# Kernel optimization log

Hardware: AMD Instinct MI355X
Metric: run time of the kernel (lower is better)

## Reference

```python
import math
import jax, jax.numpy as jnp
from jax import lax
import numpy as np

N_IMG = 2
C = 128
IMG_H, IMG_W = 512, 1024
STRIDES = (4, 8, 16, 32, 64)
SIZES = (32.0, 64.0, 128.0, 256.0, 512.0)
RATIOS = (0.5, 1.0, 2.0)
A = len(RATIOS)
PRE_NMS_TOPK = 2000    # pre_nms_topk[self.training] with training=True
POST_NMS_TOPK = 1000   # post_nms_topk[self.training]
NMS_THRESH = 0.7
BATCH_PER_IMG = 256
POS_FRAC = 0.5
MIN_BOX_SIZE = 0.0
SCALE_CLAMP = math.log(1000.0 / 16.0)
MATCH_LOW, MATCH_HIGH = 0.3, 0.7


def cell_anchors(size):
    rs = jnp.asarray(RATIOS, jnp.float32)
    area = size * size
    w = jnp.sqrt(area / rs)
    h = w * rs
    return jnp.stack([-w / 2, -h / 2, w / 2, h / 2], axis=1)  # [A,4]


def level_anchors(H, W, stride, size):
    ca = cell_anchors(size)
    sx = jnp.arange(W, dtype=jnp.float32) * stride
    sy = jnp.arange(H, dtype=jnp.float32) * stride
    yy, xx = jnp.meshgrid(sy, sx, indexing="ij")
    shifts = jnp.stack([xx, yy, xx, yy], axis=-1).reshape(-1, 4)  # [H*W,4]
    return (shifts[:, None, :] + ca[None, :, :]).reshape(-1, 4)  # [H*W*A,4]


def pairwise_iou(a, b):
    lt = jnp.maximum(a[:, None, :2], b[None, :, :2])
    rb = jnp.minimum(a[:, None, 2:], b[None, :, 2:])
    wh = jnp.clip(rb - lt, 0.0)
    inter = wh[..., 0] * wh[..., 1]
    area_a = (a[:, 2] - a[:, 0]) * (a[:, 3] - a[:, 1])
    area_b = (b[:, 2] - b[:, 0]) * (b[:, 3] - b[:, 1])
    union = area_a[:, None] + area_b[None, :] - inter
    return jnp.where(inter > 0, inter / union, 0.0)


def get_deltas(src, tgt):
    sw = src[..., 2] - src[..., 0]; sh = src[..., 3] - src[..., 1]
    scx = src[..., 0] + 0.5 * sw;   scy = src[..., 1] + 0.5 * sh
    tw = tgt[..., 2] - tgt[..., 0]; th = tgt[..., 3] - tgt[..., 1]
    tcx = tgt[..., 0] + 0.5 * tw;   tcy = tgt[..., 1] + 0.5 * th
    return jnp.stack([(tcx - scx) / sw, (tcy - scy) / sh,
                      jnp.log(tw / sw), jnp.log(th / sh)], axis=-1)


def apply_deltas(deltas, boxes):
    w = boxes[..., 2] - boxes[..., 0]; h = boxes[..., 3] - boxes[..., 1]
    cx = boxes[..., 0] + 0.5 * w;      cy = boxes[..., 1] + 0.5 * h
    dx, dy = deltas[..., 0], deltas[..., 1]
    dw = jnp.minimum(deltas[..., 2], SCALE_CLAMP)
    dh = jnp.minimum(deltas[..., 3], SCALE_CLAMP)
    pcx = dx * w + cx; pcy = dy * h + cy
    pw = jnp.exp(dw) * w; ph = jnp.exp(dh) * h
    return jnp.stack([pcx - 0.5 * pw, pcy - 0.5 * ph,
                      pcx + 0.5 * pw, pcy + 0.5 * ph], axis=-1)


def conv(x, w, b):
    y = lax.conv_general_dilated(x, w, (1, 1), "SAME",
                                 dimension_numbers=("NCHW", "OIHW", "NCHW"))
    return y + b[None, :, None, None]


def rpn_forward_flat(feats, conv_w, conv_b, obj_w, obj_b, delta_w, delta_b):
    anchors, logits, deltas = [], [], []
    for (stride, size), f in zip(zip(STRIDES, SIZES), feats):
        N, _, H, W = f.shape
        h = jax.nn.relu(conv(f, conv_w, conv_b))
        lg = conv(h, obj_w, obj_b)       # [N,A,H,W]
        dl = conv(h, delta_w, delta_b)   # [N,4A,H,W]
        logits.append(lg.transpose(0, 2, 3, 1).reshape(N, -1))                     # [N,HWA]
        deltas.append(dl.reshape(N, A, 4, H, W).transpose(0, 3, 4, 1, 2).reshape(N, -1, 4))
        anchors.append(level_anchors(H, W, stride, size))
    return anchors, logits, deltas


def label_and_sample(gt_b, key, anchors_all):
    iou = pairwise_iou(gt_b, anchors_all)                 # [G,R]
    matched_idxs = jnp.argmax(iou, axis=0)
    matched_vals = jnp.max(iou, axis=0)
    labels = jnp.where(matched_vals >= MATCH_HIGH, 1,
             jnp.where(matched_vals >= MATCH_LOW, -1, 0))
    highest = jnp.max(iou, axis=1)                        # per-gt best IoU
    lq = jnp.any((iou == highest[:, None]) & (highest[:, None] > 0), axis=0)
    labels = jnp.where(lq, 1, labels)                     # allow_low_quality_matches
    R = labels.shape[0]
    kf, kb = jax.random.split(key)
    fg = labels == 1; bg = labels == 0
    num_fg = jnp.minimum(fg.sum(), int(POS_FRAC * BATCH_PER_IMG))
    num_bg = jnp.minimum(bg.sum(), BATCH_PER_IMG - num_fg)
    def pick(mask, k, num):
        pri = jnp.where(mask, jax.random.uniform(k, (R,)), jnp.inf)
        rank = jnp.argsort(jnp.argsort(pri))
        return rank < num
    sel_fg = pick(fg, kf, num_fg)
    sel_bg = pick(bg, kb, num_bg)
    labels = jnp.where(sel_fg, 1, jnp.where(sel_bg, 0, -1))
    return labels, gt_b[matched_idxs]


def losses_fn(anchors_all, logits_cat, deltas_cat, gt_labels, matched_gt):
    fg = (gt_labels == 1).astype(logits_cat.dtype)          # [N,R]
    gt_deltas = get_deltas(anchors_all[None], matched_gt)   # [N,R,4]
    loc = jnp.sum(jnp.abs(deltas_cat - gt_deltas) * fg[..., None])  # smooth_l1, beta=0
    valid = (gt_labels >= 0).astype(logits_cat.dtype)
    x = logits_cat
    bce = jnp.maximum(x, 0.0) - x * fg + jnp.log1p(jnp.exp(-jnp.abs(x)))
    cls = jnp.sum(bce * valid)
    norm = float(BATCH_PER_IMG) * logits_cat.shape[0]
    return jnp.stack([cls / norm, loc / norm])


def nms_keep(boxes, valid):
    # boxes are sorted by descending score; greedy suppression.
    K = boxes.shape[0]
    iou = pairwise_iou(boxes, boxes)
    idx = jnp.arange(K)
    def body(i, keep):
        sup = (iou[i] > NMS_THRESH) & (idx > i) & keep[i]
        return keep & ~sup
    return lax.fori_loop(0, K, body, valid)


def predict_proposals(anchors, logits, deltas):
    lvl_boxes, lvl_scores = [], []
    for anc, lg, dl in zip(anchors, logits, deltas):
        boxes = apply_deltas(dl, anc[None])             # [N,R_l,4]
        k = min(PRE_NMS_TOPK, lg.shape[1])
        ts, ti = lax.top_k(lg, k)                       # [N,k]
        tb = jnp.take_along_axis(boxes, ti[..., None], axis=1)
        tb = jnp.stack([jnp.clip(tb[..., 0], 0.0, IMG_W), jnp.clip(tb[..., 1], 0.0, IMG_H),
                        jnp.clip(tb[..., 2], 0.0, IMG_W), jnp.clip(tb[..., 3], 0.0, IMG_H)], -1)
        valid = ((tb[..., 2] - tb[..., 0]) > MIN_BOX_SIZE) & ((tb[..., 3] - tb[..., 1]) > MIN_BOX_SIZE)
        keep = jax.vmap(nms_keep)(tb, valid)
        lvl_boxes.append(tb)
        lvl_scores.append(jnp.where(keep, ts, -jnp.inf))
    all_b = jnp.concatenate(lvl_boxes, axis=1)
    all_s = jnp.concatenate(lvl_scores, axis=1)
    fs, fi = lax.top_k(all_s, POST_NMS_TOPK)
    fb = jnp.take_along_axis(all_b, fi[..., None], axis=1)
    return fb, fs


def setup_inputs() -> dict:
    key = jax.random.key(0)
    ks = jax.random.split(key, 12)
    out = {}
    for i, s in enumerate(STRIDES):
        out[f"feat_p{i+2}"] = jax.random.normal(ks[i], (N_IMG, C, IMG_H // s, IMG_W // s), jnp.float32)
    G = 32
    wh_scale = jnp.asarray([IMG_W, IMG_H], jnp.float32)
    cxy = jax.random.uniform(ks[5], (N_IMG, G, 2)) * wh_scale
    wh = 32.0 + jax.random.uniform(ks[6], (N_IMG, G, 2)) * 224.0
    x1y1 = jnp.clip(cxy - wh / 2, 0.0)
    x2y2 = jnp.maximum(jnp.minimum(cxy + wh / 2, wh_scale), x1y1 + 1.0)
    out["gt_boxes"] = jnp.concatenate([x1y1, x2y2], axis=-1)
    out["conv_w"] = 0.01 * jax.random.normal(ks[7], (C, C, 3, 3), jnp.float32)
    out["conv_b"] = jnp.zeros((C,), jnp.float32)
    out["obj_w"] = 0.01 * jax.random.normal(ks[8], (A, C, 1, 1), jnp.float32)
    out["obj_b"] = jnp.zeros((A,), jnp.float32)
    out["delta_w"] = 0.01 * jax.random.normal(ks[9], (4 * A, C, 1, 1), jnp.float32)
    out["delta_b"] = jnp.zeros((4 * A,), jnp.float32)
    return out


def reference(feat_p2, feat_p3, feat_p4, feat_p5, feat_p6, gt_boxes,
              conv_w, conv_b, obj_w, obj_b, delta_w, delta_b):
    feats = [feat_p2, feat_p3, feat_p4, feat_p5, feat_p6]
    anchors, logits, deltas = rpn_forward_flat(feats, conv_w, conv_b, obj_w, obj_b, delta_w, delta_b)
    anchors_all = jnp.concatenate(anchors, axis=0)      # [R,4]
    logits_cat = jnp.concatenate(logits, axis=1)        # [N,R]
    deltas_cat = jnp.concatenate(deltas, axis=1)        # [N,R,4]
    keys = jax.random.split(jax.random.key(42), gt_boxes.shape[0])
    gt_labels, matched_gt = jax.vmap(label_and_sample, in_axes=(0, 0, None))(gt_boxes, keys, anchors_all)
    losses = losses_fn(anchors_all, logits_cat, deltas_cat, gt_labels, matched_gt)
    prop_boxes, prop_scores = predict_proposals(
        anchors,
        [lax.stop_gradient(l) for l in logits],
        [lax.stop_gradient(d) for d in deltas])
    return prop_boxes, prop_scores, losses
```

## Files before the change

### kernel.cpp

```cpp
#include <hip/hip_runtime.h>
#include <stdint.h>
#include <math.h>


#define R_TOT   130944
#define HALF_R  65472
#define TOTK    7920
#define SCALE_CLAMP 4.135166556742356

__host__ __device__ inline void threefry(uint32_t k0, uint32_t k1,
                                         uint32_t x0, uint32_t x1,
                                         uint32_t* o0, uint32_t* o1)
{
  uint32_t ks[3]; ks[0]=k0; ks[1]=k1; ks[2]=k0^k1^0x1BD11BDAu;
  x0 += ks[0]; x1 += ks[1];
  const uint32_t rot0[4] = {13u,15u,26u,6u};
  const uint32_t rot1[4] = {17u,29u,16u,24u};
  for (int i = 0; i < 5; i++){
    const uint32_t* rot = (i & 1) ? rot1 : rot0;
    for (int q = 0; q < 4; q++){
      x0 += x1;
      x1 = (x1 << rot[q]) | (x1 >> (32u - rot[q]));
      x1 ^= x0;
    }
    x0 += ks[(i+1)%3];
    x1 += ks[(i+2)%3] + (uint32_t)(i+1);
  }
  *o0 = x0; *o1 = x1;
}

__device__ inline unsigned long long mono64(double v){
  unsigned long long b = (unsigned long long)__double_as_longlong(v);
  return (b & 0x8000000000000000ull) ? ~b : (b | 0x8000000000000000ull);
}

__device__ __forceinline__ double iou_cf(double g0,double g1,double g2,double g3,
                                         double a0,double a1,double a2,double a3){
  #pragma clang fp contract(off)
  double lt0 = fmax(g0,a0), lt1 = fmax(g1,a1);
  double rb0 = fmin(g2,a2), rb1 = fmin(g3,a3);
  double w = rb0-lt0; if (w<0.0) w=0.0;
  double h = rb1-lt1; if (h<0.0) h=0.0;
  double inter = w*h;
  double aa = (g2-g0)*(g3-g1);
  double ab = (a2-a0)*(a3-a1);
  double uni = aa+ab-inter;
  return inter>0.0 ? inter/uni : 0.0;
}

__device__ __forceinline__ void anchor_of(int r, double* o){
  #pragma clang fp contract(off)
  const int    base[5]={0,98304,122880,129024,130560};
  const int    Wl[5]  ={256,128,64,32,16};
  const double strd[5]={4.0,8.0,16.0,32.0,64.0};
  const double size[5]={32.0,64.0,128.0,256.0,512.0};
  const double ratio[3]={0.5,1.0,2.0};
  int l=0; while (l<4 && r>=base[l+1]) l++;
  int rr=r-base[l]; int pix=rr/3; int a=rr-pix*3;
  int x=pix%Wl[l], y=pix/Wl[l];
  double w=sqrt(size[l]*size[l]/ratio[a]);
  double h=w*ratio[a];
  double sx=(double)x*strd[l], sy=(double)y*strd[l];
  o[0]=sx-0.5*w; o[1]=sy-0.5*h; o[2]=sx+0.5*w; o[3]=sy+0.5*h;
}

__device__ __forceinline__ void decode_box(int ridx, const double* __restrict__ d,
                                           double* __restrict__ o){
  double a[4]; anchor_of(ridx,a);
  double w=a[2]-a[0], h=a[3]-a[1];
  double cx=a[0]+0.5*w, cy=a[1]+0.5*h;
  double dw=fmin(d[2],SCALE_CLAMP), dh=fmin(d[3],SCALE_CLAMP);
  double pcx=d[0]*w+cx, pcy=d[1]*h+cy;
  double pw=exp(dw)*w, ph=exp(dh)*h;
  double x1=pcx-0.5*pw, y1=pcy-0.5*ph;
  double x2=pcx+0.5*pw, y2=pcy+0.5*ph;
  o[0]=fmin(fmax(x1,0.0),1024.0); o[1]=fmin(fmax(y1,0.0),512.0);
  o[2]=fmin(fmax(x2,0.0),1024.0); o[3]=fmin(fmax(y2,0.0),512.0);
}

__device__ inline void bitonic_desc(double* sv, int* si, int M, int tid, int nthr){
  for (int k=2;k<=M;k<<=1)
    for (int j=k>>1;j>0;j>>=1){
      __syncthreads();
      for (int i=tid;i<M;i+=nthr){
        int ixj=i^j;
        if (ixj>i){
          double va=sv[i], vb=sv[ixj]; int ia=si[i], ib=si[ixj];
          bool before = (va>vb) || (va==vb && ia<ib);
          bool up = ((i&k)==0);
          if (up ? !before : before){ sv[i]=vb; sv[ixj]=va; si[i]=ib; si[ixj]=ia; }
        }
      }
    }
  __syncthreads();
}

__device__ inline void bitonic_asc_u(uint32_t* sk, int* si, int M, int tid, int nthr){
  for (int k=2;k<=M;k<<=1)
    for (int j=k>>1;j>0;j>>=1){
      __syncthreads();
      for (int i=tid;i<M;i+=nthr){
        int ixj=i^j;
        if (ixj>i){
          uint32_t ka=sk[i], kb=sk[ixj]; int ia=si[i], ib=si[ixj];
          bool before = (ka<kb) || (ka==kb && ia<ib);
          bool up = ((i&k)==0);
          if (up ? !before : before){ sk[i]=kb; sk[ixj]=ka; si[i]=ib; si[ixj]=ia; }
        }
      }
    }
  __syncthreads();
}

__device__ inline void hist_select(int* hist, int kneed, int tid,
                                   int* shb, int* shk){
  for (int off=1; off<256; off<<=1){
    int v=0;
    if (tid<256 && tid>=off) v=hist[tid-off];
    __syncthreads();
    if (tid<256) hist[tid]+=v;
    __syncthreads();
  }
  if (tid<256){
    int prev = tid ? hist[tid-1] : 0;
    if (prev < kneed && kneed <= hist[tid]){ *shb=tid; *shk=kneed-prev; }
    if (tid==255 && kneed > hist[255]){ *shb=255; *shk=kneed-hist[254]; }
  }
  __syncthreads();
}

__global__ __launch_bounds__(256) void k_pre(const float* __restrict__ cw,
    float* __restrict__ cwTf, const float* __restrict__ gt,
    unsigned long long* __restrict__ highest)
{
  const int bx=blockIdx.x, tid=threadIdx.x;
  if (bx < 576){
    int o = bx*256 + tid;
    if (o >= 147456) return;
    int cc = o & 127; int t = o >> 7;
    int k9 = t % 9;  int ci = t / 9;
    cwTf[(size_t)(ci*9+k9)*128 + cc] = cw[(size_t)cc*1152 + ci*9 + k9];
  } else {
    __shared__ double gts[128];
    __shared__ unsigned long long lmax[32];
    const int gb=bx-576;
    const int img=gb>>6, b=gb&63;
    if (tid<128) gts[tid]=(double)gt[img*128+tid];
    if (tid<32) lmax[tid]=0ull;
    __syncthreads();
    double gm[32];
    #pragma unroll
    for (int g=0;g<32;g++) gm[g]=0.0;
    for (int r=b*256+tid; r<R_TOT; r+=64*256){
      double a[4]; anchor_of(r,a);
      #pragma unroll
      for (int g=0;g<32;g++){
        double v=iou_cf(gts[g*4],gts[g*4+1],gts[g*4+2],gts[g*4+3],a[0],a[1],a[2],a[3]);
        gm[g]=fmax(gm[g],v);
      }
    }
    #pragma unroll
    for (int g=0;g<32;g++){
      double v=gm[g];
      #pragma unroll
      for (int off=1; off<64; off<<=1) v=fmax(v,__shfl_xor(v,off));
      if ((tid&63)==0) atomicMax(&lmax[g],(unsigned long long)__double_as_longlong(v));
    }
    __syncthreads();
    if (tid<32) atomicMax(&highest[img*32+tid], lmax[tid]);
  }
}

#define CTH 4
#define CTW 8

__global__ __launch_bounds__(256,5) void k_conv_label(
    const float* __restrict__ f2, const float* __restrict__ f3,
    const float* __restrict__ f4, const float* __restrict__ f5,
    const float* __restrict__ f6,
    const float* __restrict__ cwTf, const float* __restrict__ cb,
    const float* __restrict__ ow, const float* __restrict__ ob,
    const float* __restrict__ dwt, const float* __restrict__ dbt,
    double* __restrict__ logits, double* __restrict__ dpred,
    const float* __restrict__ gt, const unsigned long long* __restrict__ highest,
    int* __restrict__ prelab, int* __restrict__ matched,
    int* __restrict__ labels, int* __restrict__ counts,
    uint32_t* __restrict__ ub,
    uint32_t kf00,uint32_t kf01,uint32_t kb00,uint32_t kb01,
    uint32_t kf10,uint32_t kf11,uint32_t kb10,uint32_t kb11)
{
  __shared__ double fshd[4][6][12];
  __shared__ __align__(16) char ush[18432];
  float*  wshF = (float*)ush;
  double* hshp = (double*)ush;
  __shared__ float hw[15*128];
  __shared__ float hb[15];

  const int tid=threadIdx.x;

  if (blockIdx.x >= 3752){
    int j = (blockIdx.x-3752)*256 + tid;
    if (j >= 2*R_TOT) return;
    int slot = j / HALF_R; int t = j - slot*HALF_R;
    uint32_t k0,k1;
    if      (slot==0){k0=kf00;k1=kf01;}
    else if (slot==1){k0=kb00;k1=kb01;}
    else if (slot==2){k0=kf10;k1=kf11;}
    else             {k0=kb10;k1=kb11;}
    uint32_t o0,o1;
    threefry(k0,k1,(uint32_t)t,(uint32_t)(t+HALF_R),&o0,&o1);
    ub[(size_t)slot*R_TOT+t]=o0;
    ub[(size_t)slot*R_TOT+t+HALF_R]=o1;
    return;
  }

  if (blockIdx.x >= 2728){
    double* gts=(double*)ush;
    double* hg =(double*)(ush+1024);
    int* wfg=(int*)(ush+1280); int* wbg=(int*)(ush+1296);
    const int lb=blockIdx.x-2728;
    const int img=lb>>9, blk=lb&511;
    if (tid<128) gts[tid]=(double)gt[img*128+tid];
    if (tid<32)  hg[tid]=__longlong_as_double((long long)highest[img*32+tid]);
    __syncthreads();
    int r=blk*256+tid;
    const bool ok=(r<R_TOT);
    int lab=-1, bi=0;
    if (ok){
      double a[4]; anchor_of(r,a);
      double best=-1.0; bool lq=false;
      #pragma unroll
      for (int g=0;g<32;g++){
        double v=iou_cf(gts[g*4],gts[g*4+1],gts[g*4+2],gts[g*4+3],a[0],a[1],a[2],a[3]);
        if (v>best){ best=v; bi=g; }
        if (hg[g]>0.0 && v==hg[g]) lq=true;
      }
      lab = lq ? 1 : (best>=0.7 ? 1 : (best>=0.3 ? -1 : 0));
      prelab [(size_t)img*R_TOT+r]=lab;
      matched[(size_t)img*R_TOT+r]=bi;
      labels [(size_t)img*R_TOT+r]=-1;
    }
    unsigned long long bf=__ballot(ok && lab==1);
    unsigned long long bb=__ballot(ok && lab==0);
    const int wid=tid>>6, lane=tid&63;
    if (lane==0){ wfg[wid]=__popcll(bf); wbg[wid]=__popcll(bb); }
    __syncthreads();
    if (tid==0){
      int fcnt=wfg[0]+wfg[1]+wfg[2]+wfg[3];
      int bcnt=wbg[0]+wbg[1]+wbg[2]+wbg[3];
      if (fcnt) atomicAdd(&counts[img*2+0],fcnt);
      if (bcnt) atomicAdd(&counts[img*2+1],bcnt);
    }
    return;
  }

  const int cumt[6]={0,2048,2560,2688,2720,2728};
  const int Hs[5]={128,64,32,16,8}, Wl[5]={256,128,64,32,16};
  const int rbs[5]={0,98304,122880,129024,130560};
  const int lgx[5]={5,4,3,2,1};

  int bid=blockIdx.x;
  int lvl=0;
  while (lvl<4 && bid>=cumt[lvl+1]) lvl++;
  int t=bid-cumt[lvl];
  const int img=t&1; const int tt=t>>1;
  const int H=Hs[lvl], W=Wl[lvl], rbase=rbs[lvl];
  const int tx=tt&((1<<lgx[lvl])-1), ty=tt>>lgx[lvl];
  const int x0=tx*CTW, y0=ty*CTH;
  const float* f = lvl==0?f2: lvl==1?f3: lvl==2?f4: lvl==3?f5: f6;

  for (int i=tid;i<15*128;i+=256){
    int o=i>>7, c=i&127;
    hw[i]=(o<3)?ow[o*128+c]:dwt[(o-3)*128+c];
  }
  if (tid<15) hb[tid]=(tid<3)?ob[tid]:dbt[tid-3];

  const int c=tid&127, half=tid>>7;
  double acc[16];
  #pragma unroll
  for (int i=0;i<16;i++) acc[i]=0.0;

  const float* fimg = f + (size_t)img*128*H*W;

  const bool fin_act = (tid < 240);
  int ci_f=0,dy_f=0,dx_f=0; bool fin_valid=false;
  const float* fptr=fimg;
  if (fin_act){
    ci_f=tid/60; int rem=tid-ci_f*60; dy_f=rem/10; dx_f=rem-dy_f*10;
    int y=y0-1+dy_f, x=x0-1+dx_f;
    fin_valid = (y>=0&&y<H&&x>=0&&x<W);
    fptr = fimg + (size_t)ci_f*H*W + (fin_valid ? ((size_t)y*W+x) : 0);
  }
  const size_t fstep=(size_t)4*H*W;
  const float2* wsrc=(const float2*)cwTf;

  float fin_pf=0.f; float2 wpf[9];
  if (fin_act){ fin_pf = fin_valid ? *fptr : 0.f; fptr += fstep; }
  #pragma unroll
  for (int j2=0;j2<9;j2++) wpf[j2]=wsrc[tid+j2*256];

  for (int ci0=0; ci0<128; ci0+=4){
    __syncthreads();
    if (fin_act) fshd[ci_f][dy_f][dx_f]=(double)fin_pf;
    { float2* wdst=(float2*)wshF;
      #pragma unroll
      for (int j2=0;j2<9;j2++) wdst[tid+j2*256]=wpf[j2]; }
    if (ci0+4<128){
      if (fin_act){ fin_pf = fin_valid ? *fptr : 0.f; fptr += fstep; }
      const float2* wn = wsrc + (size_t)(ci0+4)*576;
      #pragma unroll
      for (int j2=0;j2<9;j2++) wpf[j2]=wn[tid+j2*256];
    }
    __syncthreads();
    #pragma unroll
    for (int ci=0;ci<4;ci++){
      double w9d[9];
      #pragma unroll
      for (int k=0;k<9;k++) w9d[k]=(double)wshF[(ci*9+k)*128 + c];
      #pragma unroll
      for (int irl=0;irl<4;irl++){
        int ir=half*2+irl;
        double rowb[10];
        #pragma unroll
        for (int q=0;q<10;q++) rowb[q]=fshd[ci][ir][q];
        #pragma unroll
        for (int orl=0;orl<2;orl++){
          int ky=irl-orl;
          if (ky<0||ky>2) continue;
          #pragma unroll
          for (int px=0;px<8;px++){
            double s=acc[orl*8+px];
            #pragma unroll
            for (int kx=0;kx<3;kx++) s += w9d[ky*3+kx]*rowb[px+kx];
            acc[orl*8+px]=s;
          }
        }
      }
    }
  }
  double bc=(double)cb[c];
  __syncthreads();
  if (half==0){
    #pragma unroll
    for (int pp=0;pp<16;pp++){
      double hv=acc[pp]+bc; if (hv<0.0) hv=0.0;
      hshp[c*17+pp]=hv;
    }
  }
  __syncthreads();
  for (int hp=0;hp<2;hp++){
    if (tid<240){
      int o=tid>>4, p=tid&15;
      double s=(double)hb[o];
      for (int c2=0;c2<128;c2++) s += (double)hw[o*128+c2]*hshp[c2*17+p];
      int pg=hp*16+p;
      int py=pg>>3, px=pg&7;
      int gy=y0+py, gx=x0+px;
      long long pix=(long long)gy*W+gx;
      size_t rb=(size_t)rbase+(size_t)pix*3;
      if (o<3) logits[(size_t)img*R_TOT+rb+o]=s;
      else { int a=(o-3)>>2, jj=(o-3)&3; dpred[((size_t)img*R_TOT+rb+a)*4+jj]=s; }
    }
    if (hp==0){
      __syncthreads();
      if (half==1){
        #pragma unroll
        for (int pp=0;pp<16;pp++){
          double hv=acc[pp]+bc; if (hv<0.0) hv=0.0;
          hshp[c*17+pp]=hv;
        }
      }
      __syncthreads();
    }
  }
}

__global__ __launch_bounds__(1024) void k_mid2(const uint32_t* __restrict__ ub,
    const int* __restrict__ prelab, const int* __restrict__ counts,
    int* __restrict__ labels,
    const double* __restrict__ logits, const double* __restrict__ dpred,
    double* __restrict__ allS, double* __restrict__ allB)
{
  __shared__ __align__(16) char buf[49152];
  __shared__ int hist[256];
  __shared__ int sI0, sI1;
  __shared__ int cnt;
  const int tid=threadIdx.x;

  if (blockIdx.x < 4){
    uint32_t* skey=(uint32_t*)buf; int* sidx=(int*)(buf+16384);
    const int img=blockIdx.x>>1, cls=blockIdx.x&1;
    const int cfg=counts[img*2+0], cbg=counts[img*2+1];
    const int num_fg=cfg<128?cfg:128;
    const int cap_bg=256-num_fg;
    const int num=cls?(cbg<cap_bg?cbg:cap_bg):num_fg;
    if (num<=0) return;
    const int want=cls?0:1;
    const int sel=want;
    const uint32_t* u=ub+(size_t)(img*2+cls)*R_TOT;
    const int* pl=prelab+(size_t)img*R_TOT;
    int* lab=labels+(size_t)img*R_TOT;

    for (int b=tid;b<256;b+=1024) hist[b]=0;
    if (tid==0) cnt=0;
    __syncthreads();
    for (int r=tid;r<R_TOT;r+=1024){
      int plr = pl[r];
      uint32_t key = u[r]>>9;
      if (plr==want) atomicAdd(&hist[key>>15],1);
    }
    __syncthreads();
    hist_select(hist, num, tid, &sI0, &sI1);
    const uint32_t bsel=(uint32_t)sI0; const int kneed=sI1;
    for (int r=tid;r<R_TOT;r+=1024){
      int plr = pl[r];
      uint32_t key = u[r]>>9;
      if (plr==want){
        uint32_t t8=key>>15;
        if (t8<bsel) lab[r]=sel;
        else if (t8==bsel){ int p=atomicAdd(&cnt,1); if (p<4096){ skey[p]=key; sidx[p]=r; } }
      }
    }
    __syncthreads();
    int n=cnt<4096?cnt:4096;
    for (int i=tid;i<4096;i+=1024) if (i>=n){ skey[i]=0xFFFFFFFFu; sidx[i]=0x7FFFFFFF; }
    bitonic_asc_u(skey,sidx,4096,tid,1024);
    int take = kneed<n?kneed:n;
    for (int i=tid;i<take;i+=1024) lab[sidx[i]]=sel;
  } else {
    double* sv=(double*)buf; int* si=(int*)(buf+32768);
    const int Rl[5]   ={98304,24576,6144,1536,384};
    const int kl[5]   ={2000,2000,2000,1536,384};
    const int lbase[5]={0,98304,122880,129024,130560};
    const int loff[5] ={0,2000,4000,6000,7536};
    const int bb=blockIdx.x-4;
    const int lvl=bb%5, img=bb/5;
    const int Rn=Rl[lvl], K=kl[lvl];
    const double* lg=logits+(size_t)img*R_TOT+lbase[lvl];

    unsigned long long chosen=0; int kneed=K;
    for (int ps=7; ps>=6; --ps){
      int shift=ps*8;
      for (int b=tid;b<256;b+=1024) hist[b]=0;
      __syncthreads();
      for (int r=tid;r<Rn;r+=1024){
        unsigned long long ik=~mono64(lg[r]);
        bool okp=(ps==7)||((ik>>(shift+8))==(chosen>>(shift+8)));
        if (okp) atomicAdd(&hist[(int)((ik>>shift)&255)],1);
      }
      __syncthreads();
      hist_select(hist, kneed, tid, &sI0, &sI1);
      chosen = chosen | ((unsigned long long)sI0<<shift);
      kneed  = sI1;
      __syncthreads();
    }
    const unsigned long long lim = chosen | 0xFFFFFFFFFFFFull;
    if (tid==0) cnt=0;
    __syncthreads();
    for (int r=tid;r<Rn;r+=1024){
      unsigned long long ik=~mono64(lg[r]);
      if (ik<=lim){ int p=atomicAdd(&cnt,1); if (p<4096){ sv[p]=lg[r]; si[p]=r; } }
    }
    __syncthreads();
    int n=cnt<4096?cnt:4096;
    for (int i=tid;i<4096;i+=1024) if (i>=n){ sv[i]=-HUGE_VAL; si[i]=0x7FFFFFFF; }
    bitonic_desc(sv,si,4096,tid,1024);
    for (int j=tid;j<K;j+=1024){
      double v=sv[j]; int r=si[j];
      size_t slot=(size_t)img*TOTK+loff[lvl]+j;
      allS[slot]=v;
      int ridx=lbase[lvl]+r;
      double bx[4];
      decode_box(ridx, dpred+((size_t)img*R_TOT+ridx)*4, bx);
      allB[slot*4+0]=bx[0]; allB[slot*4+1]=bx[1]; allB[slot*4+2]=bx[2]; allB[slot*4+3]=bx[3];
    }
  }
}

__global__ __launch_bounds__(256) void k_mid3(const double* __restrict__ allB,
    unsigned long long* __restrict__ msk,
    const double* __restrict__ logits, const double* __restrict__ dpred,
    const float* __restrict__ gt, const int* __restrict__ labels,
    const int* __restrict__ matched, double* __restrict__ part)
{
  const int bx=blockIdx.x, tid=threadIdx.x;
  if (bx < 1980){
    __shared__ double Bsh[8000];
    const int kl[5]  ={2000,2000,2000,1536,384};
    const int loff[5]={0,2000,4000,6000,7536};
    const int rbc[6] ={0,250,500,750,942,990};
    const int img = bx/990; int t = bx - img*990;
    int lvl=0; while (lvl<4 && t>=rbc[lvl+1]) lvl++;
    const int i0=(t-rbc[lvl])*8;
    const int K=kl[lvl]; const int nw=(K+63)>>6;
    const double* B=allB+(size_t)(img*TOTK+loff[lvl])*4;
    for (int q=tid;q<K*4;q+=256) Bsh[q]=B[q];
    __syncthreads();
    const int wv=tid>>6, lane=tid&63;
    for (int rr=0;rr<8;rr++){
      int i=i0+rr;
      if (i>=K) break;
      const double bi0=Bsh[i*4],bi1=Bsh[i*4+1],bi2=Bsh[i*4+2],bi3=Bsh[i*4+3];
      const double areai=(bi2-bi0)*(bi3-bi1);
      for (int w=wv;w<nw;w+=4){
        int j=w*64+lane;
        bool pred=false;
        if (j<K && j>i){
          double a0=Bsh[j*4],a1=Bsh[j*4+1],a2=Bsh[j*4+2],a3=Bsh[j*4+3];
          double lt0=fmax(bi0,a0), lt1=fmax(bi1,a1);
          double rb0=fmin(bi2,a2), rb1=fmin(bi3,a3);
          double ww=rb0-lt0; if (ww<0.0) ww=0.0;
          double hh=rb1-lt1; if (hh<0.0) hh=0.0;
          double inter=ww*hh;
          double uni=areai+(a2-a0)*(a3-a1)-inter;
          double iou=inter>0.0?inter/uni:0.0;
          pred = iou>0.7;
        }
        unsigned long long m=__ballot(pred);
        if (lane==0) msk[((size_t)img*TOTK+loff[lvl]+i)*32+w]=m;
      }
    }
  } else {
    const int bid2=bx-1980;
    double cls=0.0, loc=0.0;
    for (int idx=bid2*256+tid; idx<2*R_TOT; idx+=256*256){
      int l=labels[idx];
      if (l<0) continue;
      double x=logits[idx];
      double fgv=(l==1)?1.0:0.0;
      cls += fmax(x,0.0)-x*fgv+log1p(exp(-fabs(x)));
      if (l==1){
        int img=idx/R_TOT, r=idx-img*R_TOT;
        double a[4]; anchor_of(r,a);
        int m=matched[idx];
        const float* g=gt+img*128+m*4;
        double sw=a[2]-a[0], sh=a[3]-a[1];
        double scx=a[0]+0.5*sw, scy=a[1]+0.5*sh;
        double tw=(double)g[2]-(double)g[0], th=(double)g[3]-(double)g[1];
        double tcx=(double)g[0]+0.5*tw, tcy=(double)g[1]+0.5*th;
        double d0=(tcx-scx)/sw, d1=(tcy-scy)/sh;
        double d2=log(tw/sw), d3=log(th/sh);
        const double* dp=dpred+(size_t)idx*4;
        loc += fabs(dp[0]-d0)+fabs(dp[1]-d1)+fabs(dp[2]-d2)+fabs(dp[3]-d3);
      }
    }
    __shared__ double sc[256], sl[256];
    sc[tid]=cls; sl[tid]=loc; __syncthreads();
    for (int s=128;s>0;s>>=1){
      if (tid<s){ sc[tid]+=sc[tid+s]; sl[tid]+=sl[tid+s]; }
      __syncthreads();
    }
    if (tid==0){ part[bid2*2]=sc[0]; part[bid2*2+1]=sl[0]; }
  }
}

#define NMS_LD(BUF, BASE) do{ \
  _Pragma("unroll") \
  for (int j_=0;j_<16;j_++){ int i_=(BASE)+j_; \
    BUF[j_] = (lane<nw && i_<K) ? M[(size_t)i_*32+lane] : 0ull; } \
}while(0)
#define NMS_PR(BUF, BASE) do{ \
  _Pragma("unroll") \
  for (int j_=0;j_<16;j_++){ int i_=(BASE)+j_; \
    if (i_<K){ unsigned long long kw_=__shfl(keep,(i_>>6)); \
      if ((kw_>>(i_&63))&1ull) keep &= ~BUF[j_]; } } \
}while(0)

__global__ void k_nmsscan(const double* __restrict__ allB, double* __restrict__ allS,
    const unsigned long long* __restrict__ msk){
  const int kl[5]  ={2000,2000,2000,1536,384};
  const int loff[5]={0,2000,4000,6000,7536};
  const int lvl=blockIdx.x, img=blockIdx.y;
  const int K=kl[lvl], off=loff[lvl], nw=(K+63)>>6;
  const int lane=threadIdx.x;
  const double* B=allB+(size_t)(img*TOTK+off)*4;
  const unsigned long long* M=msk+((size_t)img*TOTK+off)*32;
  unsigned long long keep=0ull;
  if (lane<nw){
    for (int b=0;b<64;b++){
      int j=lane*64+b;
      if (j<K){
        double x1=B[(size_t)j*4],y1=B[(size_t)j*4+1],x2=B[(size_t)j*4+2],y2=B[(size_t)j*4+3];
        if ((x2-x1)>0.0 && (y2-y1)>0.0) keep|=(1ull<<b);
      }
    }
  }
  unsigned long long Abuf[16], Bbuf[16];
  NMS_LD(Abuf, 0);
  for (int base=0; base<K; base+=32){
    NMS_LD(Bbuf, base+16);
    NMS_PR(Abuf, base);
    NMS_LD(Abuf, base+32);
    NMS_PR(Bbuf, base+16);
  }
  if (lane<nw){
    for (int b=0;b<64;b++){
      int j=lane*64+b;
      if (j<K && !((keep>>b)&1ull))
        allS[(size_t)img*TOTK+off+j]=-HUGE_VAL;
    }
  }
}

__global__ __launch_bounds__(1024) void k_final(const double* __restrict__ allS,
    const double* __restrict__ allB, const double* __restrict__ part,
    float* __restrict__ out){
  const int tid=threadIdx.x;
  if (blockIdx.x==2){
    __shared__ double sc[256], sl[256];
    if (tid<256){ sc[tid]=part[tid*2]; sl[tid]=part[tid*2+1]; }
    __syncthreads();
    for (int s=128;s>0;s>>=1){
      if (tid<s){ sc[tid]+=sc[tid+s]; sl[tid]+=sl[tid+s]; }
      __syncthreads();
    }
    if (tid==0){ out[10000]=(float)(sc[0]/512.0); out[10001]=(float)(sl[0]/512.0); }
    return;
  }
  const int img=blockIdx.x;
  const double* sarr=allS+(size_t)img*TOTK;
  __shared__ int hist[256];
  __shared__ int sI0, sI1;
  __shared__ double sv[4096]; __shared__ int si[4096]; __shared__ int cnt;

  unsigned long long chosen=0; int kneed=1000;
  for (int ps=7; ps>=6; --ps){
    int shift=ps*8;
    for (int b=tid;b<256;b+=1024) hist[b]=0;
    __syncthreads();
    for (int r=tid;r<TOTK;r+=1024){
      unsigned long long ik=~mono64(sarr[r]);
      bool okp=(ps==7)||((ik>>(shift+8))==(chosen>>(shift+8)));
      if (okp) atomicAdd(&hist[(int)((ik>>shift)&255)],1);
    }
    __syncthreads();
    hist_select(hist, kneed, tid, &sI0, &sI1);
    chosen = chosen | ((unsigned long long)sI0<<shift);
    kneed  = sI1;
    __syncthreads();
  }
  const unsigned long long lim = chosen | 0xFFFFFFFFFFFFull;
  if (tid==0) cnt=0;
  __syncthreads();
  for (int r=tid;r<TOTK;r+=1024){
    unsigned long long ik=~mono64(sarr[r]);
    if (ik<=lim){ int p=atomicAdd(&cnt,1); if (p<4096){ sv[p]=sarr[r]; si[p]=r; } }
  }
  __syncthreads();
  int n=cnt<4096?cnt:4096;
  for (int i=tid;i<4096;i+=1024) if (i>=n){ sv[i]=-HUGE_VAL; si[i]=0x7FFFFFFF; }
  bitonic_desc(sv,si,4096,tid,1024);
  for (int j=tid;j<1000;j+=1024){
    out[8000+img*1000+j]=(float)sv[j];
    int idx=si[j];
    const double* b=allB+((size_t)img*TOTK+idx)*4;
    float* ob=out+((size_t)img*1000+j)*4;
    ob[0]=(float)b[0]; ob[1]=(float)b[1]; ob[2]=(float)b[2]; ob[3]=(float)b[3];
  }
}

extern "C" void kernel_launch(void* const* d_in, const int* in_sizes, int n_in,
                              void* d_out, int out_size, void* d_ws, size_t ws_size,
                              hipStream_t stream)
{
  (void)in_sizes; (void)n_in; (void)out_size;
  const float* feats[5];
  for (int i=0;i<5;i++) feats[i]=(const float*)d_in[i];
  const float* gt =(const float*)d_in[5];
  const float* cw =(const float*)d_in[6];
  const float* cb =(const float*)d_in[7];
  const float* ow =(const float*)d_in[8];
  const float* ob =(const float*)d_in[9];
  const float* dwt=(const float*)d_in[10];
  const float* dbt=(const float*)d_in[11];
  float* out=(float*)d_out;

  char* p=(char*)d_ws;
  auto carve=[&](size_t nbytes)->char*{ char* q=p; p += (nbytes+255)&~(size_t)255; return q; };
  double* logits =(double*)carve(2ull*R_TOT*8);
  double* dpred  =(double*)carve(2ull*R_TOT*4*8);
  float* cwTf    =(float*)carve(147456ull*4);
  uint32_t* ub   =(uint32_t*)carve(4ull*R_TOT*4);
  int* prelab    =(int*)carve(2ull*R_TOT*4);
  int* matched   =(int*)carve(2ull*R_TOT*4);
  int* labels    =(int*)carve(2ull*R_TOT*4);
  unsigned long long* highest=(unsigned long long*)carve(2*32*8);
  int* counts    =(int*)carve(256);
  double* allS   =(double*)carve(2ull*TOTK*8);
  double* allB   =(double*)carve(2ull*TOTK*4*8);
  unsigned long long* msk=(unsigned long long*)carve(2ull*TOTK*32*8);
  double* part   =(double*)carve(256*2*8);
  if ((size_t)(p-(char*)d_ws) > ws_size) return;

  hipMemsetAsync(highest, 0, 768, stream);

  uint32_t a0,b0,a1,b1;
  threefry(0u,42u,0u,2u,&a0,&b0);
  threefry(0u,42u,1u,3u,&a1,&b1);
  uint32_t kf00,kf01,kb00,kb01,kf10,kf11,kb10,kb11;
  { uint32_t c0,d0,c1,d1;
    threefry(a0,a1,0u,2u,&c0,&d0); threefry(a0,a1,1u,3u,&c1,&d1);
    kf00=c0; kf01=c1; kb00=d0; kb01=d1;
    threefry(b0,b1,0u,2u,&c0,&d0); threefry(b0,b1,1u,3u,&c1,&d1);
    kf10=c0; kf11=c1; kb10=d0; kb11=d1; }

  k_pre<<<704, 256, 0, stream>>>(cw, cwTf, gt, highest);
  k_conv_label<<<4775, 256, 0, stream>>>(feats[0],feats[1],feats[2],feats[3],feats[4],
      cwTf,cb,ow,ob,dwt,dbt, logits, dpred,
      gt, highest, prelab, matched, labels, counts,
      ub, kf00,kf01,kb00,kb01,kf10,kf11,kb10,kb11);
  k_mid2<<<14, 1024, 0, stream>>>(ub, prelab, counts, labels, logits, dpred, allS, allB);
  k_mid3<<<2236, 256, 0, stream>>>(allB, msk, logits, dpred, gt, labels, matched, part);
  k_nmsscan<<<dim3(5,2), 64, 0, stream>>>(allB, allS, msk);
  k_final<<<3, 1024, 0, stream>>>(allS, allB, part, out);
}
```

Measured before the change: 1.354 ms.

## Fuse NMS scan and final top-k into one kernel using flag-synchronised blocks

The separate NMS-scan and final-selection kernels are merged into one launch, k_post. Ten blocks run the per-level NMS bit scan and clear suppressed bits in a global keep bitmask with atomicAnd, then bump a per-image flag. Two blocks spin-wait on that flag and do the top-1000 selection from the masked scores, and one block does the loss reduction. The goal is to remove a kernel launch and the write-back of -inf scores. Separately, the conv/label kernel's launch-bounds occupancy hint drops from 5 to 3 blocks, and several scan loops in k_mid2 get unroll-4 pragmas. The spin-wait is only safe because all 13 blocks can be resident at once.

```diff
diff --git a/kernel.cpp b/kernel.cpp
--- a/kernel.cpp
+++ b/kernel.cpp
@@ -174,7 +174,7 @@
 #define CTH 4
 #define CTW 8
 
-__global__ __launch_bounds__(256,5) void k_conv_label(
+__global__ __launch_bounds__(256,3) void k_conv_label(
     const float* __restrict__ f2, const float* __restrict__ f3,
     const float* __restrict__ f4, const float* __restrict__ f5,
     const float* __restrict__ f6,
@@ -379,7 +379,8 @@
     const int* __restrict__ prelab, const int* __restrict__ counts,
     int* __restrict__ labels,
     const double* __restrict__ logits, const double* __restrict__ dpred,
-    double* __restrict__ allS, double* __restrict__ allB)
+    double* __restrict__ allS, double* __restrict__ allB,
+    unsigned long long* __restrict__ keepbuf)
 {
   __shared__ __align__(16) char buf[49152];
   __shared__ int hist[256];
@@ -404,6 +405,7 @@
     for (int b=tid;b<256;b+=1024) hist[b]=0;
     if (tid==0) cnt=0;
     __syncthreads();
+    #pragma unroll 4
     for (int r=tid;r<R_TOT;r+=1024){
       int plr = pl[r];
       uint32_t key = u[r]>>9;
@@ -412,6 +414,7 @@
     __syncthreads();
     hist_select(hist, num, tid, &sI0, &sI1);
     const uint32_t bsel=(uint32_t)sI0; const int kneed=sI1;
+    #pragma unroll 4
     for (int r=tid;r<R_TOT;r+=1024){
       int plr = pl[r];
       uint32_t key = u[r]>>9;
@@ -435,6 +438,7 @@
     const int loff[5] ={0,2000,4000,6000,7536};
     const int bb=blockIdx.x-4;
     const int lvl=bb%5, img=bb/5;
+    if (lvl==0 && tid<124) keepbuf[img*124+tid]=~0ull;
     const int Rn=Rl[lvl], K=kl[lvl];
     const double* lg=logits+(size_t)img*R_TOT+lbase[lvl];
 
@@ -443,6 +447,7 @@
       int shift=ps*8;
       for (int b=tid;b<256;b+=1024) hist[b]=0;
       __syncthreads();
+      #pragma unroll 4
       for (int r=tid;r<Rn;r+=1024){
         unsigned long long ik=~mono64(lg[r]);
         bool okp=(ps==7)||((ik>>(shift+8))==(chosen>>(shift+8)));
@@ -457,6 +462,7 @@
     const unsigned long long lim = chosen | 0xFFFFFFFFFFFFull;
     if (tid==0) cnt=0;
     __syncthreads();
+    #pragma unroll 4
     for (int r=tid;r<Rn;r+=1024){
       unsigned long long ik=~mono64(lg[r]);
       if (ik<=lim){ int p=atomicAdd(&cnt,1); if (p<4096){ sv[p]=lg[r]; si[p]=r; } }
@@ -566,97 +572,125 @@
       if ((kw_>>(i_&63))&1ull) keep &= ~BUF[j_]; } } \
 }while(0)
 
-__global__ void k_nmsscan(const double* __restrict__ allB, double* __restrict__ allS,
-    const unsigned long long* __restrict__ msk){
+__global__ __launch_bounds__(1024) void k_post(const double* __restrict__ allB,
+    const double* __restrict__ allS, const unsigned long long* __restrict__ msk,
+    const double* __restrict__ part, int* __restrict__ flags,
+    unsigned long long* __restrict__ keepbuf, float* __restrict__ out)
+{
+  const int tid=threadIdx.x, bx=blockIdx.x;
   const int kl[5]  ={2000,2000,2000,1536,384};
   const int loff[5]={0,2000,4000,6000,7536};
-  const int lvl=blockIdx.x, img=blockIdx.y;
-  const int K=kl[lvl], off=loff[lvl], nw=(K+63)>>6;
-  const int lane=threadIdx.x;
-  const double* B=allB+(size_t)(img*TOTK+off)*4;
-  const unsigned long long* M=msk+((size_t)img*TOTK+off)*32;
-  unsigned long long keep=0ull;
-  if (lane<nw){
-    for (int b=0;b<64;b++){
-      int j=lane*64+b;
-      if (j<K){
-        double x1=B[(size_t)j*4],y1=B[(size_t)j*4+1],x2=B[(size_t)j*4+2],y2=B[(size_t)j*4+3];
-        if ((x2-x1)>0.0 && (y2-y1)>0.0) keep|=(1ull<<b);
-      }
-    }
-  }
-  unsigned long long Abuf[16], Bbuf[16];
-  NMS_LD(Abuf, 0);
-  for (int base=0; base<K; base+=32){
-    NMS_LD(Bbuf, base+16);
-    NMS_PR(Abuf, base);
-    NMS_LD(Abuf, base+32);
-    NMS_PR(Bbuf, base+16);
-  }
-  if (lane<nw){
-    for (int b=0;b<64;b++){
-      int j=lane*64+b;
-      if (j<K && !((keep>>b)&1ull))
-        allS[(size_t)img*TOTK+off+j]=-HUGE_VAL;
-    }
-  }
-}
-
-__global__ __launch_bounds__(1024) void k_final(const double* __restrict__ allS,
-    const double* __restrict__ allB, const double* __restrict__ part,
-    float* __restrict__ out){
-  const int tid=threadIdx.x;
-  if (blockIdx.x==2){
-    __shared__ double sc[256], sl[256];
-    if (tid<256){ sc[tid]=part[tid*2]; sl[tid]=part[tid*2+1]; }
-    __syncthreads();
-    for (int s=128;s>0;s>>=1){
-      if (tid<s){ sc[tid]+=sc[tid+s]; sl[tid]+=sl[tid+s]; }
-      __syncthreads();
-    }
-    if (tid==0){ out[10000]=(float)(sc[0]/512.0); out[10001]=(float)(sl[0]/512.0); }
+
+  if (bx < 10){
+    if (tid >= 64) return;
+    const int lvl=bx%5, img=bx/5;
+    const int K=kl[lvl], off=loff[lvl], nw=(K+63)>>6;
+    const int lane=tid;
+    const double* B=allB+(size_t)(img*TOTK+off)*4;
+    const unsigned long long* M=msk+((size_t)img*TOTK+off)*32;
+    unsigned long long keep=0ull;
+    if (lane<nw){
+      for (int b=0;b<64;b++){
+        int j=lane*64+b;
+        if (j<K){
+          double x1=B[(size_t)j*4],y1=B[(size_t)j*4+1],x2=B[(size_t)j*4+2],y2=B[(size_t)j*4+3];
+          if ((x2-x1)>0.0 && (y2-y1)>0.0) keep|=(1ull<<b);
+        }
+      }
+    }
+    unsigned long long Abuf[16], Bbuf[16];
+    NMS_LD(Abuf, 0);
+    for (int base=0; base<K; base+=32){
+      NMS_LD(Bbuf, base+16);
+      NMS_PR(Abuf, base);
+      NMS_LD(Abuf, base+32);
+      NMS_PR(Bbuf, base+16);
+    }
+    if (lane<nw){
+      int nvalid = K - lane*64; if (nvalid>64) nvalid=64;
+      unsigned long long vm = (nvalid>=64) ? ~0ull : ((1ull<<nvalid)-1ull);
+      unsigned long long cbits = (~keep) & vm;
+      int gbase = off + lane*64;
+      int w0 = gbase>>6, sh = gbase&63;
+      unsigned long long* kb = keepbuf + (size_t)img*124;
+      if (sh==0){
+        if (cbits) atomicAnd(&kb[w0], ~cbits);
+      } else {
+        unsigned long long lo = cbits << sh;
+        unsigned long long hi = cbits >> (64-sh);
+        if (lo) atomicAnd(&kb[w0],   ~lo);
+        if (hi) atomicAnd(&kb[w0+1], ~hi);
+      }
+    }
+    __threadfence();
+    if (tid==0) atomicAdd(&flags[img],1);
     return;
   }
-  const int img=blockIdx.x;
-  const double* sarr=allS+(size_t)img*TOTK;
-  __shared__ int hist[256];
-  __shared__ int sI0, sI1;
-  __shared__ double sv[4096]; __shared__ int si[4096]; __shared__ int cnt;
-
-  unsigned long long chosen=0; int kneed=1000;
-  for (int ps=7; ps>=6; --ps){
-    int shift=ps*8;
-    for (int b=tid;b<256;b+=1024) hist[b]=0;
+
+  if (bx < 12){
+    const int img=bx-10;
+    if (tid==0){
+      while (atomicAdd(&flags[img],0) < 5) __builtin_amdgcn_s_sleep(8);
+    }
+    __syncthreads();
+    __threadfence();
+    __shared__ unsigned long long kbl[124];
+    if (tid<124) kbl[tid]=atomicAdd(&keepbuf[(size_t)img*124+tid],0ull);
+    __syncthreads();
+    const double* sarr=allS+(size_t)img*TOTK;
+    __shared__ int hist[256];
+    __shared__ int sI0, sI1;
+    __shared__ double sv[4096]; __shared__ int si[4096]; __shared__ int cnt;
+
+    unsigned long long chosen=0; int kneed=1000;
+    for (int ps=7; ps>=6; --ps){
+      int shift=ps*8;
+      for (int b=tid;b<256;b+=1024) hist[b]=0;
+      __syncthreads();
+      for (int r=tid;r<TOTK;r+=1024){
+        bool kept = (kbl[r>>6]>>(r&63))&1ull;
+        double val = kept ? sarr[r] : -HUGE_VAL;
+        unsigned long long ik=~mono64(val);
+        bool okp=(ps==7)||((ik>>(shift+8))==(chosen>>(shift+8)));
+        if (okp) atomicAdd(&hist[(int)((ik>>shift)&255)],1);
+      }
+      __syncthreads();
+      hist_select(hist, kneed, tid, &sI0, &sI1);
+      chosen = chosen | ((unsigned long long)sI0<<shift);
+      kneed  = sI1;
+      __syncthreads();
+    }
+    const unsigned long long lim = chosen | 0xFFFFFFFFFFFFull;
+    if (tid==0) cnt=0;
     __syncthreads();
     for (int r=tid;r<TOTK;r+=1024){
-      unsigned long long ik=~mono64(sarr[r]);
-      bool okp=(ps==7)||((ik>>(shift+8))==(chosen>>(shift+8)));
-      if (okp) atomicAdd(&hist[(int)((ik>>shift)&255)],1);
-    }
-    __syncthreads();
-    hist_select(hist, kneed, tid, &sI0, &sI1);
-    chosen = chosen | ((unsigned long long)sI0<<shift);
-    kneed  = sI1;
-    __syncthreads();
-  }
-  const unsigned long long lim = chosen | 0xFFFFFFFFFFFFull;
-  if (tid==0) cnt=0;
+      bool kept = (kbl[r>>6]>>(r&63))&1ull;
+      double val = kept ? sarr[r] : -HUGE_VAL;
+      unsigned long long ik=~mono64(val);
+      if (ik<=lim){ int p=atomicAdd(&cnt,1); if (p<4096){ sv[p]=val; si[p]=r; } }
+    }
+    __syncthreads();
+    int n=cnt<4096?cnt:4096;
+    for (int i=tid;i<4096;i+=1024) if (i>=n){ sv[i]=-HUGE_VAL; si[i]=0x7FFFFFFF; }
+    bitonic_desc(sv,si,4096,tid,1024);
+    for (int j=tid;j<1000;j+=1024){
+      out[8000+img*1000+j]=(float)sv[j];
+      int idx=si[j];
+      const double* b=allB+((size_t)img*TOTK+idx)*4;
+      float* ob=out+((size_t)img*1000+j)*4;
+      ob[0]=(float)b[0]; ob[1]=(float)b[1]; ob[2]=(float)b[2]; ob[3]=(float)b[3];
+    }
+    return;
+  }
+
+  __shared__ double sc[256], sl[256];
+  if (tid<256){ sc[tid]=part[tid*2]; sl[tid]=part[tid*2+1]; }
   __syncthreads();
-  for (int r=tid;r<TOTK;r+=1024){
-    unsigned long long ik=~mono64(sarr[r]);
-    if (ik<=lim){ int p=atomicAdd(&cnt,1); if (p<4096){ sv[p]=sarr[r]; si[p]=r; } }
-  }
-  __syncthreads();
-  int n=cnt<4096?cnt:4096;
-  for (int i=tid;i<4096;i+=1024) if (i>=n){ sv[i]=-HUGE_VAL; si[i]=0x7FFFFFFF; }
-  bitonic_desc(sv,si,4096,tid,1024);
-  for (int j=tid;j<1000;j+=1024){
-    out[8000+img*1000+j]=(float)sv[j];
-    int idx=si[j];
-    const double* b=allB+((size_t)img*TOTK+idx)*4;
-    float* ob=out+((size_t)img*1000+j)*4;
-    ob[0]=(float)b[0]; ob[1]=(float)b[1]; ob[2]=(float)b[2]; ob[3]=(float)b[3];
-  }
+  for (int s=128;s>0;s>>=1){
+    if (tid<s){ sc[tid]+=sc[tid+s]; sl[tid]+=sl[tid+s]; }
+    __syncthreads();
+  }
+  if (tid==0){ out[10000]=(float)(sc[0]/512.0); out[10001]=(float)(sl[0]/512.0); }
 }
 
 extern "C" void kernel_launch(void* const* d_in, const int* in_sizes, int n_in,
@@ -686,13 +720,15 @@
   int* labels    =(int*)carve(2ull*R_TOT*4);
   unsigned long long* highest=(unsigned long long*)carve(2*32*8);
   int* counts    =(int*)carve(256);
+  int* flags     =(int*)carve(256);
   double* allS   =(double*)carve(2ull*TOTK*8);
   double* allB   =(double*)carve(2ull*TOTK*4*8);
   unsigned long long* msk=(unsigned long long*)carve(2ull*TOTK*32*8);
   double* part   =(double*)carve(256*2*8);
+  unsigned long long* keepbuf=(unsigned long long*)carve(2*124*8);
   if ((size_t)(p-(char*)d_ws) > ws_size) return;
 
-  hipMemsetAsync(highest, 0, 768, stream);
+  hipMemsetAsync(highest, 0, 1024, stream);
 
   uint32_t a0,b0,a1,b1;
   threefry(0u,42u,0u,2u,&a0,&b0);
@@ -709,8 +745,7 @@
       cwTf,cb,ow,ob,dwt,dbt, logits, dpred,
       gt, highest, prelab, matched, labels, counts,
       ub, kf00,kf01,kb00,kb01,kf10,kf11,kb10,kb11);
-  k_mid2<<<14, 1024, 0, stream>>>(ub, prelab, counts, labels, logits, dpred, allS, allB);
+  k_mid2<<<14, 1024, 0, stream>>>(ub, prelab, counts, labels, logits, dpred, allS, allB, keepbuf);
   k_mid3<<<2236, 256, 0, stream>>>(allB, msk, logits, dpred, gt, labels, matched, part);
-  k_nmsscan<<<dim3(5,2), 64, 0, stream>>>(allB, allS, msk);
-  k_final<<<3, 1024, 0, stream>>>(allS, allB, part, out);
-}
+  k_post<<<13, 1024, 0, stream>>>(allB, allS, msk, part, flags, keepbuf, out);
+}
```

New measurement: 1.343 ms. Within noise of the previous version (-0.8%).
